# Optimization experiments

Measured on AMD Instinct MI355X. Metric: run time of the kernel, lower is better.

## Reference

```python
import jax, jax.numpy as jnp
import numpy as np

IN_DIM, HID, D_PK = 6, 64, 64
B, T = 256, 2048
EPS = 1e-5


def setup_inputs() -> dict:
    key = jax.random.key(0)
    ks = jax.random.split(key, 12)
    s_in = 1.0 / np.sqrt(IN_DIM)
    s_h = 1.0 / np.sqrt(HID)
    return {
        "drug_ce": jax.random.normal(ks[0], (B, T, IN_DIM), dtype=jnp.float32),
        "w1": jax.random.uniform(ks[1], (IN_DIM, HID), minval=-s_in, maxval=s_in, dtype=jnp.float32),
        "b1": jax.random.uniform(ks[2], (HID,), minval=-s_in, maxval=s_in, dtype=jnp.float32),
        "ln1_g": jnp.ones((HID,), jnp.float32),
        "ln1_b": jnp.zeros((HID,), jnp.float32),
        "W_ih": jax.random.uniform(ks[3], (3 * HID, HID), minval=-s_h, maxval=s_h, dtype=jnp.float32),
        "b_ih": jax.random.uniform(ks[4], (3 * HID,), minval=-s_h, maxval=s_h, dtype=jnp.float32),
        "W_hh": jax.random.uniform(ks[5], (3 * HID, HID), minval=-s_h, maxval=s_h, dtype=jnp.float32),
        "b_hh": jax.random.uniform(ks[6], (3 * HID,), minval=-s_h, maxval=s_h, dtype=jnp.float32),
        "w2": jax.random.uniform(ks[7], (HID, D_PK), minval=-s_h, maxval=s_h, dtype=jnp.float32),
        "b2": jax.random.uniform(ks[8], (D_PK,), minval=-s_h, maxval=s_h, dtype=jnp.float32),
        "ln2_g": jnp.ones((D_PK,), jnp.float32),
        "ln2_b": jnp.zeros((D_PK,), jnp.float32),
    }


def _layernorm(x, g, b):
    m = jnp.mean(x, axis=-1, keepdims=True)
    v = jnp.mean(jnp.square(x - m), axis=-1, keepdims=True)
    return (x - m) * jax.lax.rsqrt(v + EPS) * g + b


def reference(drug_ce, w1, b1, ln1_g, ln1_b, W_ih, b_ih, W_hh, b_hh, w2, b2, ln2_g, ln2_b):
    # input_proj: Linear -> LayerNorm -> GELU (exact, erf-based as in torch)
    x = jax.nn.gelu(_layernorm(drug_ce @ w1 + b1, ln1_g, ln1_b), approximate=False)  # (B,T,H)

    # Precompute input-side gate pre-activations for all timesteps
    gi = jnp.einsum('bth,gh->btg', x, W_ih) + b_ih  # (B,T,3H)
    gi_t = jnp.swapaxes(gi, 0, 1)  # (T,B,3H)

    h0 = jnp.zeros((drug_ce.shape[0], HID), dtype=drug_ce.dtype)

    def step(h, gi_step):
        gh = h @ W_hh.T + b_hh  # (B,3H)
        i_r, i_z, i_n = jnp.split(gi_step, 3, axis=-1)
        h_r, h_z, h_n = jnp.split(gh, 3, axis=-1)
        r = jax.nn.sigmoid(i_r + h_r)
        z = jax.nn.sigmoid(i_z + h_z)
        n = jnp.tanh(i_n + r * h_n)
        h_new = (1.0 - z) * n + z * h
        return h_new, h_new

    _, h_seq_t = jax.lax.scan(step, h0, gi_t)  # (T,B,H)
    h_seq = jnp.swapaxes(h_seq_t, 0, 1)  # (B,T,H)

    # out_proj: Linear -> LayerNorm
    return _layernorm(h_seq @ w2 + b2, ln2_g, ln2_b)
```

## Files before the change

kernel.cpp:

```cpp
#include <hip/hip_runtime.h>
#include <math.h>

#define HID 64
#define TST 2048
#define CH 16
#define NCH (TST / CH)
#define EPSN 1e-5f

typedef float v2f __attribute__((ext_vector_type(2)));

#define REP32(M) M(0) M(1) M(2) M(3) M(4) M(5) M(6) M(7) \
                 M(8) M(9) M(10) M(11) M(12) M(13) M(14) M(15) \
                 M(16) M(17) M(18) M(19) M(20) M(21) M(22) M(23) \
                 M(24) M(25) M(26) M(27) M(28) M(29) M(30) M(31)

__global__ void k_inproj(const float* __restrict__ ce, const float* __restrict__ w1,
                         const float* __restrict__ b1, const float* __restrict__ g1,
                         const float* __restrict__ be1, float* __restrict__ xout,
                         int nrows) {
    const int lane = threadIdx.x & 63;
    const int wave = threadIdx.x >> 6;
    const long row = (long)blockIdx.x * 4 + wave;
    if (row >= nrows) return;
    const float* cr = ce + row * 6;
    float acc = b1[lane];
    acc += cr[0] * w1[0 * HID + lane];
    acc += cr[1] * w1[1 * HID + lane];
    acc += cr[2] * w1[2 * HID + lane];
    acc += cr[3] * w1[3 * HID + lane];
    acc += cr[4] * w1[4 * HID + lane];
    acc += cr[5] * w1[5 * HID + lane];
    float s = acc;
#pragma unroll
    for (int m = 32; m >= 1; m >>= 1) s += __shfl_xor(s, m, 64);
    const float mean = s * (1.0f / 64.0f);
    const float d = acc - mean;
    float q = d * d;
#pragma unroll
    for (int m = 32; m >= 1; m >>= 1) q += __shfl_xor(q, m, 64);
    const float var = q * (1.0f / 64.0f);
    const float xn = d * rsqrtf(var + EPSN) * g1[lane] + be1[lane];
    const float ge = 0.5f * xn * (1.0f + erff(xn * 0.70710678118654752440f));
    xout[row * HID + lane] = ge;
}

__device__ __forceinline__ float gru_step(float gr, float gz, float gn,
                                          float pr, float pz, float pn, float h) {
    const float r = 1.0f / (1.0f + __expf(-(gr + pr)));
    const float z = 1.0f / (1.0f + __expf(-(gz + pz)));
    const float pre = gn + r * pn;
    const float e2 = __expf(2.0f * pre);
    const float n = 1.0f - 2.0f / (e2 + 1.0f);
    return (1.0f - z) * n + z * h;
}

__global__ __launch_bounds__(512, 2)
void k_gru(float* xo,
           const float* __restrict__ W_ih, const float* __restrict__ b_ih,
           const float* __restrict__ W_hh, const float* __restrict__ b_hh,
           const float* __restrict__ w2, const float* __restrict__ b2,
           const float* __restrict__ g2, const float* __restrict__ be2) {
    __shared__ __align__(16) float4 xbuf[2][CH][16];
    __shared__ __align__(16) float gibuf[2][CH][192];
    __shared__ __align__(16) float hist[4][CH][HID];
    __shared__ __align__(16) float hb[3][HID];
    __shared__ __align__(16) float part[2][3][HID];
    __shared__ __align__(16) float ybuf[2][8][HID];

    const int tid = threadIdx.x;
    const int lane = tid & 63;
    const int wv = tid >> 6;
    float* xb = xo + (size_t)blockIdx.x * TST * HID;

#define DECLW(i) v2f W##i = {0.f, 0.f};
    REP32(DECLW)
    float bh = 0.f, b2r = 0.f, g2r = 0.f, be2r = 0.f;

    if (wv < 6) {
        const float* wbp = (wv < 3) ? (W_hh + (size_t)(wv * 64 + lane) * HID)
                                    : (W_ih + (size_t)((wv - 3) * 64 + lane) * HID);
        const v2f* r0 = (const v2f*)wbp;
#define LWR(i) W##i = r0[i];
        REP32(LWR)
        bh = (wv < 3) ? b_hh[wv * 64 + lane] : b_ih[(wv - 3) * 64 + lane];
    } else if (wv == 6) {
#define LW6(i) W##i.x = w2[(size_t)(2 * (i)) * HID + lane]; \
               W##i.y = w2[(size_t)(2 * (i) + 1) * HID + lane];
        REP32(LW6)
        b2r = b2[lane]; g2r = g2[lane]; be2r = be2[lane];
    }
#define PINW(i) asm volatile("" : "+a"(W##i));
    REP32(PINW)

    if (tid < 256) ((float4*)&xbuf[0][0][0])[tid] = ((const float4*)xb)[tid];
    if (wv < 3) part[0][wv][lane] = bh;
    float h_reg = 0.f;
    float pown = bh;
    __syncthreads();

#define MACH(i) { const v2f u = hv[i]; if ((i) & 1) a1 += W##i * u; else a0 += W##i * u; }
#define MACX(i) { const v2f u = xv[i]; if ((i) & 1) a1 += W##i * u; else a0 += W##i * u; }
#define MACE(i) { const v2f u = hr[i]; if ((i) & 1) a1 += W##i * u; else a0 += W##i * u; }

#define LNR4(slot, ub, chk, rbase) { \
    float yv[4], sv[4], qv[4]; \
    _Pragma("unroll") for (int u = 0; u < 4; ++u) yv[u] = ybuf[slot][(ub) + u][lane]; \
    _Pragma("unroll") for (int u = 0; u < 4; ++u) { sv[u] = yv[u]; qv[u] = yv[u] * yv[u]; } \
    _Pragma("unroll") for (int m = 32; m >= 1; m >>= 1) { \
        _Pragma("unroll") for (int u = 0; u < 4; ++u) sv[u] += __shfl_xor(sv[u], m, 64); \
        _Pragma("unroll") for (int u = 0; u < 4; ++u) qv[u] += __shfl_xor(qv[u], m, 64); } \
    _Pragma("unroll") for (int u = 0; u < 4; ++u) { \
        const float mean = sv[u] * (1.0f / 64.0f); \
        const float var = qv[u] * (1.0f / 64.0f) - mean * mean; \
        const float dd = yv[u] - mean; \
        xb[(size_t)((chk) * CH + (rbase) + u) * HID + lane] = \
            dd * rsqrtf(var + EPSN) * g2r + be2r; } }

    for (int s = -16; s <= 2081; ++s) {
        const int c = s >> 4;
        const int t = s & 15;
        if (wv < 3) {
            if (s >= 0 && s < TST) {
                const float* gp = &gibuf[c & 1][t][0];
                const float gr = gp[lane], gz = gp[64 + lane], gn = gp[128 + lane];
                float pr, pz, pn;
                if (wv == 0)      { pr = pown;                   pz = part[s & 1][1][lane]; pn = part[s & 1][2][lane]; }
                else if (wv == 1) { pr = part[s & 1][0][lane];   pz = pown;                 pn = part[s & 1][2][lane]; }
                else              { pr = part[s & 1][0][lane];   pz = part[s & 1][1][lane]; pn = pown; }
                h_reg = gru_step(gr, gz, gn, pr, pz, pn, h_reg);
                hb[wv][lane] = h_reg;
                const v2f* hv = (const v2f*)&hb[wv][0];
                v2f a0 = {0.f, 0.f}, a1 = {0.f, 0.f};
                REP32(MACH)
                const v2f av = a0 + a1;
                pown = av.x + av.y + bh;
                part[(s + 1) & 1][wv][lane] = pown;
            }
        } else if (wv < 6) {
            if (s < TST - CH) {
                const int sf = s + CH;
                const v2f* xv = (const v2f*)&xbuf[(sf >> 4) & 1][sf & 15][0];
                v2f a0 = {0.f, 0.f}, a1 = {0.f, 0.f};
                REP32(MACX)
                const v2f av = a0 + a1;
                gibuf[(sf >> 4) & 1][sf & 15][(wv - 3) * 64 + lane] = av.x + av.y + bh;
            }
        } else if (wv == 6) {
            if (s >= 32 && c <= 129) {
                const v2f* hr = (const v2f*)&hist[(c - 2) & 3][t][0];
                v2f a0 = {0.f, 0.f}, a1 = {0.f, 0.f};
                REP32(MACE)
                const v2f av = a0 + a1;
                ybuf[t >> 3][t & 7][lane] = b2r + av.x + av.y;
            }
            if ((t == 8 || t == 9) && c >= 2 && c <= 129) {
                const int ub = (t - 8) * 4;
                LNR4(0, ub, c - 2, ub)
            }
            if ((t == 0 || t == 1) && c >= 3 && c <= 130) {
                const int ub = t * 4;
                LNR4(1, ub, c - 3, 8 + ub)
            }
        } else {
            if (s >= 0 && s < TST) {
                const float* gp = &gibuf[c & 1][t][0];
                const float pr = part[s & 1][0][lane];
                const float pz = part[s & 1][1][lane];
                const float pn = part[s & 1][2][lane];
                h_reg = gru_step(gp[lane], gp[64 + lane], gp[128 + lane], pr, pz, pn, h_reg);
                hist[c & 3][t][lane] = h_reg;
            }
            if (t == 0 && c >= -1 && c <= 125) {
                const float4* src = (const float4*)(xb + (size_t)(c + 2) * CH * HID);
                float4* dst = (float4*)&xbuf[c & 1][0][0];
#pragma unroll
                for (int q = 0; q < 4; ++q) dst[lane + q * 64] = src[lane + q * 64];
            }
        }
        __syncthreads();
    }
}

extern "C" void kernel_launch(void* const* d_in, const int* in_sizes, int n_in,
                              void* d_out, int out_size, void* d_ws, size_t ws_size,
                              hipStream_t stream) {
    const float* ce  = (const float*)d_in[0];
    const float* w1  = (const float*)d_in[1];
    const float* b1  = (const float*)d_in[2];
    const float* g1  = (const float*)d_in[3];
    const float* be1 = (const float*)d_in[4];
    const float* Wih = (const float*)d_in[5];
    const float* bih = (const float*)d_in[6];
    const float* Whh = (const float*)d_in[7];
    const float* bhh = (const float*)d_in[8];
    const float* w2  = (const float*)d_in[9];
    const float* b2  = (const float*)d_in[10];
    const float* g2  = (const float*)d_in[11];
    const float* be2 = (const float*)d_in[12];
    float* out = (float*)d_out;

    const int nrows = in_sizes[0] / 6;
    const int B = nrows / TST;

    k_inproj<<<(nrows + 3) / 4, 256, 0, stream>>>(ce, w1, b1, g1, be1, out, nrows);
    k_gru<<<B, 512, 0, stream>>>(out, Wih, bih, Whh, bhh, w2, b2, g2, be2);
}
```

Baseline: 1.725 ms.

## Broadcast hidden state via readlane instead of LDS, defer prefetch store

The recurrent matvec no longer writes h to shared memory and reads it back as v2f vectors. Each lane keeps its own h element and the full vector is built with 64 readlane broadcasts feeding scalar FMAs into four accumulators. The same pattern replaces the LDS vector reads in the input-projection and output-projection waves. The global prefetch of the next x chunk now loads into registers at t==0 and writes to LDS at t==4, so the load latency is hidden across steps. This removes an LDS round trip on the serial critical path, at the cost of losing packed v2f math and issuing 64 readlanes per step.

New measurement: 2.034 ms. 1.18x slower.

```diff
diff --git a/kernel.cpp b/kernel.cpp
--- a/kernel.cpp
+++ b/kernel.cpp
@@ -7,12 +7,11 @@
 #define NCH (TST / CH)
 #define EPSN 1e-5f
 
-typedef float v2f __attribute__((ext_vector_type(2)));
-
-#define REP32(M) M(0) M(1) M(2) M(3) M(4) M(5) M(6) M(7) \
-                 M(8) M(9) M(10) M(11) M(12) M(13) M(14) M(15) \
-                 M(16) M(17) M(18) M(19) M(20) M(21) M(22) M(23) \
-                 M(24) M(25) M(26) M(27) M(28) M(29) M(30) M(31)
+#define REP64(M) \
+  M(0) M(1) M(2) M(3) M(4) M(5) M(6) M(7) M(8) M(9) M(10) M(11) M(12) M(13) M(14) M(15) \
+  M(16) M(17) M(18) M(19) M(20) M(21) M(22) M(23) M(24) M(25) M(26) M(27) M(28) M(29) M(30) M(31) \
+  M(32) M(33) M(34) M(35) M(36) M(37) M(38) M(39) M(40) M(41) M(42) M(43) M(44) M(45) M(46) M(47) \
+  M(48) M(49) M(50) M(51) M(52) M(53) M(54) M(55) M(56) M(57) M(58) M(59) M(60) M(61) M(62) M(63)
 
 __global__ void k_inproj(const float* __restrict__ ce, const float* __restrict__ w1,
                          const float* __restrict__ b1, const float* __restrict__ g1,
@@ -63,7 +62,6 @@
     __shared__ __align__(16) float4 xbuf[2][CH][16];
     __shared__ __align__(16) float gibuf[2][CH][192];
     __shared__ __align__(16) float hist[4][CH][HID];
-    __shared__ __align__(16) float hb[3][HID];
     __shared__ __align__(16) float part[2][3][HID];
     __shared__ __align__(16) float ybuf[2][8][HID];
 
@@ -72,35 +70,36 @@
     const int wv = tid >> 6;
     float* xb = xo + (size_t)blockIdx.x * TST * HID;
 
-#define DECLW(i) v2f W##i = {0.f, 0.f};
-    REP32(DECLW)
+#define DECLW(j) float W##j = 0.f;
+    REP64(DECLW)
     float bh = 0.f, b2r = 0.f, g2r = 0.f, be2r = 0.f;
 
     if (wv < 6) {
         const float* wbp = (wv < 3) ? (W_hh + (size_t)(wv * 64 + lane) * HID)
                                     : (W_ih + (size_t)((wv - 3) * 64 + lane) * HID);
-        const v2f* r0 = (const v2f*)wbp;
-#define LWR(i) W##i = r0[i];
-        REP32(LWR)
+#define LWR(j) W##j = wbp[j];
+        REP64(LWR)
         bh = (wv < 3) ? b_hh[wv * 64 + lane] : b_ih[(wv - 3) * 64 + lane];
     } else if (wv == 6) {
-#define LW6(i) W##i.x = w2[(size_t)(2 * (i)) * HID + lane]; \
-               W##i.y = w2[(size_t)(2 * (i) + 1) * HID + lane];
-        REP32(LW6)
+#define LW6(j) W##j = w2[(size_t)(j) * HID + lane];
+        REP64(LW6)
         b2r = b2[lane]; g2r = g2[lane]; be2r = be2[lane];
     }
-#define PINW(i) asm volatile("" : "+a"(W##i));
-    REP32(PINW)
+#define PINW(j) asm volatile("" : "+a"(W##j));
+    REP64(PINW)
 
     if (tid < 256) ((float4*)&xbuf[0][0][0])[tid] = ((const float4*)xb)[tid];
     if (wv < 3) part[0][wv][lane] = bh;
     float h_reg = 0.f;
     float pown = bh;
+    float4 pf0 = {0,0,0,0}, pf1 = {0,0,0,0}, pf2 = {0,0,0,0}, pf3 = {0,0,0,0};
     __syncthreads();
 
-#define MACH(i) { const v2f u = hv[i]; if ((i) & 1) a1 += W##i * u; else a0 += W##i * u; }
-#define MACX(i) { const v2f u = xv[i]; if ((i) & 1) a1 += W##i * u; else a0 += W##i * u; }
-#define MACE(i) { const v2f u = hr[i]; if ((i) & 1) a1 += W##i * u; else a0 += W##i * u; }
+#define MACJ(j) { const float hj = __int_as_float(__builtin_amdgcn_readlane(hsI, j)); \
+                  if (((j) & 3) == 0)      a0 = fmaf(hj, W##j, a0); \
+                  else if (((j) & 3) == 1) a1 = fmaf(hj, W##j, a1); \
+                  else if (((j) & 3) == 2) a2 = fmaf(hj, W##j, a2); \
+                  else                     a3 = fmaf(hj, W##j, a3); }
 
 #define LNR4(slot, ub, chk, rbase) { \
     float yv[4], sv[4], qv[4]; \
@@ -124,34 +123,33 @@
                 const float* gp = &gibuf[c & 1][t][0];
                 const float gr = gp[lane], gz = gp[64 + lane], gn = gp[128 + lane];
                 float pr, pz, pn;
-                if (wv == 0)      { pr = pown;                   pz = part[s & 1][1][lane]; pn = part[s & 1][2][lane]; }
-                else if (wv == 1) { pr = part[s & 1][0][lane];   pz = pown;                 pn = part[s & 1][2][lane]; }
-                else              { pr = part[s & 1][0][lane];   pz = part[s & 1][1][lane]; pn = pown; }
+                if (wv == 0)      { pr = pown;                 pz = part[s & 1][1][lane]; pn = part[s & 1][2][lane]; }
+                else if (wv == 1) { pr = part[s & 1][0][lane]; pz = pown;                 pn = part[s & 1][2][lane]; }
+                else              { pr = part[s & 1][0][lane]; pz = part[s & 1][1][lane]; pn = pown; }
                 h_reg = gru_step(gr, gz, gn, pr, pz, pn, h_reg);
-                hb[wv][lane] = h_reg;
-                const v2f* hv = (const v2f*)&hb[wv][0];
-                v2f a0 = {0.f, 0.f}, a1 = {0.f, 0.f};
-                REP32(MACH)
-                const v2f av = a0 + a1;
-                pown = av.x + av.y + bh;
+                const int hsI = __float_as_int(h_reg);
+                float a0 = 0.f, a1 = 0.f, a2 = 0.f, a3 = 0.f;
+                REP64(MACJ)
+                pown = ((a0 + a1) + (a2 + a3)) + bh;
                 part[(s + 1) & 1][wv][lane] = pown;
             }
         } else if (wv < 6) {
             if (s < TST - CH) {
                 const int sf = s + CH;
-                const v2f* xv = (const v2f*)&xbuf[(sf >> 4) & 1][sf & 15][0];
-                v2f a0 = {0.f, 0.f}, a1 = {0.f, 0.f};
-                REP32(MACX)
-                const v2f av = a0 + a1;
-                gibuf[(sf >> 4) & 1][sf & 15][(wv - 3) * 64 + lane] = av.x + av.y + bh;
+                const float xr = ((const float*)&xbuf[(sf >> 4) & 1][sf & 15][0])[lane];
+                const int hsI = __float_as_int(xr);
+                float a0 = 0.f, a1 = 0.f, a2 = 0.f, a3 = 0.f;
+                REP64(MACJ)
+                gibuf[(sf >> 4) & 1][sf & 15][(wv - 3) * 64 + lane] =
+                    ((a0 + a1) + (a2 + a3)) + bh;
             }
         } else if (wv == 6) {
             if (s >= 32 && c <= 129) {
-                const v2f* hr = (const v2f*)&hist[(c - 2) & 3][t][0];
-                v2f a0 = {0.f, 0.f}, a1 = {0.f, 0.f};
-                REP32(MACE)
-                const v2f av = a0 + a1;
-                ybuf[t >> 3][t & 7][lane] = b2r + av.x + av.y;
+                const float hrow = hist[(c - 2) & 3][t][lane];
+                const int hsI = __float_as_int(hrow);
+                float a0 = 0.f, a1 = 0.f, a2 = 0.f, a3 = 0.f;
+                REP64(MACJ)
+                ybuf[t >> 3][t & 7][lane] = b2r + ((a0 + a1) + (a2 + a3));
             }
             if ((t == 8 || t == 9) && c >= 2 && c <= 129) {
                 const int ub = (t - 8) * 4;
@@ -172,9 +170,13 @@
             }
             if (t == 0 && c >= -1 && c <= 125) {
                 const float4* src = (const float4*)(xb + (size_t)(c + 2) * CH * HID);
+                pf0 = src[lane]; pf1 = src[lane + 64];
+                pf2 = src[lane + 128]; pf3 = src[lane + 192];
+            }
+            if (t == 4 && c >= -1 && c <= 125) {
                 float4* dst = (float4*)&xbuf[c & 1][0][0];
-#pragma unroll
-                for (int q = 0; q < 4; ++q) dst[lane + q * 64] = src[lane + q * 64];
+                dst[lane] = pf0; dst[lane + 64] = pf1;
+                dst[lane + 128] = pf2; dst[lane + 192] = pf3;
             }
         }
         __syncthreads();
```
